# Kernel tuning notes

Hardware: AMD Instinct MI355X
Metric: run time of the kernel (lower is better)

## Reference

```python
import jax, jax.numpy as jnp
import numpy as np

H = 32  # hidden size

def _lstm_layer(x, Wih, Whh, bih, bhh):
    # x: [B, T, in]; Wih: [4H, in]; Whh: [4H, H]; biases: [4H]
    # Precompute input contribution for all timesteps (one big GEMM).
    xg = jnp.einsum('bti,gi->btg', x, Wih) + (bih + bhh)  # [B, T, 4H]
    B = x.shape[0]
    h0 = jnp.zeros((B, H), x.dtype)
    c0 = jnp.zeros((B, H), x.dtype)

    def step(carry, xt):
        h, c = carry
        g = xt + h @ Whh.T                      # [B, 4H]
        i, f, gg, o = jnp.split(g, 4, axis=-1)   # PyTorch gate order: i,f,g,o
        i = jax.nn.sigmoid(i)
        f = jax.nn.sigmoid(f)
        gg = jnp.tanh(gg)
        o = jax.nn.sigmoid(o)
        c = f * c + i * gg
        h = o * jnp.tanh(c)
        return (h, c), h

    (_, _), hs = jax.lax.scan(step, (h0, c0), jnp.swapaxes(xg, 0, 1))  # hs: [T, B, H]
    return jnp.swapaxes(hs, 0, 1)  # [B, T, H]


def setup_inputs() -> dict:
    key = jax.random.key(0)
    ks = jax.random.split(key, 11)
    B, T = 4096, 1024
    s = 1.0 / np.sqrt(H)  # PyTorch LSTM init scale
    f32 = jnp.float32
    return {
        'x':    jax.random.normal(ks[0], (B, T, 1), dtype=f32),
        'Wih0': jax.random.uniform(ks[1], (4 * H, 1), dtype=f32, minval=-s, maxval=s),
        'Whh0': jax.random.uniform(ks[2], (4 * H, H), dtype=f32, minval=-s, maxval=s),
        'bih0': jax.random.uniform(ks[3], (4 * H,), dtype=f32, minval=-s, maxval=s),
        'bhh0': jax.random.uniform(ks[4], (4 * H,), dtype=f32, minval=-s, maxval=s),
        'Wih1': jax.random.uniform(ks[5], (4 * H, H), dtype=f32, minval=-s, maxval=s),
        'Whh1': jax.random.uniform(ks[6], (4 * H, H), dtype=f32, minval=-s, maxval=s),
        'bih1': jax.random.uniform(ks[7], (4 * H,), dtype=f32, minval=-s, maxval=s),
        'bhh1': jax.random.uniform(ks[8], (4 * H,), dtype=f32, minval=-s, maxval=s),
        'Wfc':  jax.random.uniform(ks[9], (1, H), dtype=f32, minval=-s, maxval=s),
        'bfc':  jax.random.uniform(ks[10], (1,), dtype=f32, minval=-s, maxval=s),
    }


def reference(x, Wih0, Whh0, bih0, bhh0, Wih1, Whh1, bih1, bhh1, Wfc, bfc):
    h1 = _lstm_layer(x, Wih0, Whh0, bih0, bhh0)   # [B, T, H]
    h2 = _lstm_layer(h1, Wih1, Whh1, bih1, bhh1)  # [B, T, H]
    last = h2[:, -1, :]                            # [B, H]
    return last @ Wfc.T + bfc                      # [B, 1]
```

## Files before the change

kernel.cpp:

```cpp
#include <hip/hip_runtime.h>

#define HSZ  32
#define TLEN 1024
#define PS   40

typedef _Float16 half8 __attribute__((ext_vector_type(8)));
typedef float    f32x4 __attribute__((ext_vector_type(4)));

__device__ __forceinline__ float rcp_f(float x){ return __builtin_amdgcn_rcpf(x); }
__device__ __forceinline__ float exp2_f(float x){ return __builtin_amdgcn_exp2f(x); }
#define LOG2E 1.442695040888963f
__device__ __forceinline__ float sigmoid_f(float x){ return rcp_f(1.0f + exp2_f(-LOG2E*x)); }
__device__ __forceinline__ float tanh_fast(float x){ return 1.0f - 2.0f*rcp_f(1.0f + exp2_f(2.0f*LOG2E*x)); }
__device__ __forceinline__ f32x4 mfma16(half8 a, half8 b, f32x4 c){
  return __builtin_amdgcn_mfma_f32_16x16x32_f16(a, b, c, 0, 0, 0);
}

__device__ __forceinline__ void lds_barrier(){
  asm volatile("s_waitcnt lgkmcnt(0)\n\ts_barrier" ::: "memory");
}

__global__ __launch_bounds__(512, 2) void lstm2_mfma8(
    const float* __restrict__ x,
    const float* __restrict__ Wih0, const float* __restrict__ Whh0,
    const float* __restrict__ bih0, const float* __restrict__ bhh0,
    const float* __restrict__ Wih1, const float* __restrict__ Whh1,
    const float* __restrict__ bih1, const float* __restrict__ bhh1,
    const float* __restrict__ Wfc,  const float* __restrict__ bfc,
    float* __restrict__ out, int Tn)
{
  __shared__ __align__(16) _Float16 hpl[2][2][16*PS];

  const int tid = threadIdx.x;
  const int w   = tid >> 6;
  const int l   = tid & 63;
  const int col = l & 15;
  const int g   = l >> 4;
  const int s   = 4*w + g;
  const int b0  = blockIdx.x * 16;

  const int prow = 32*(col & 3) + 4*w + (col >> 2);
  half8 W0h, W0l, WIh, WIl, WHh, WHl;
  {
    const float* p0 = Whh0 + prow*HSZ + 8*g;
    const float* p1 = Wih1 + prow*HSZ + 8*g;
    const float* p2 = Whh1 + prow*HSZ + 8*g;
    #pragma unroll
    for (int j = 0; j < 8; ++j){
      float v0 = p0[j], v1 = p1[j], v2 = p2[j];
      _Float16 a = (_Float16)v0; W0h[j] = a; W0l[j] = (_Float16)(v0 - (float)a);
      _Float16 b = (_Float16)v1; WIh[j] = b; WIl[j] = (_Float16)(v1 - (float)b);
      _Float16 c = (_Float16)v2; WHh[j] = c; WHl[j] = (_Float16)(v2 - (float)c);
    }
  }
  float wx[4], bs0[4];
  f32x4 bias1;
  #pragma unroll
  for (int j = 0; j < 4; ++j){
    int r    = 32*j + s;
    wx[j]    = Wih0[r];
    bs0[j]   = bih0[r] + bhh0[r];
    bias1[j] = bih1[r] + bhh1[r];
  }
  const f32x4 zero4 = {0.f, 0.f, 0.f, 0.f};

  const int wrI = col*PS + s;
  const int rdI = col*PS + 8*g;

  for (int i = tid; i < 2*2*16*PS; i += 512) (&hpl[0][0][0])[i] = (_Float16)0.0f;

  const float* xp = x + (size_t)(b0 + col) * Tn;
  float c0, c1 = 0.f, h1v = 0.f;

  {
    float x0 = xp[0];
    float e0 = fmaf(x0, wx[0], bs0[0]);
    float e2 = fmaf(x0, wx[2], bs0[2]);
    float e3 = fmaf(x0, wx[3], bs0[3]);
    float i0 = sigmoid_f(e0);
    float g0 = tanh_fast(e2);
    float o0 = sigmoid_f(e3);
    c0 = i0 * g0;
    float h0 = o0 * tanh_fast(c0);
    __syncthreads();
    hpl[0][0][wrI] = (_Float16)h0;
  }
  __syncthreads();
  half8 Bh0 = *(const half8*)&hpl[0][0][rdI];
  half8 Bh1 = *(const half8*)&hpl[0][1][rdI];
  float xv = xp[1];

#define STEP(Q, TIDX)                                                      \
  {                                                                        \
    float xn = xp[(TIDX)];               \
    f32x4 e;                                                               \
    e[0] = fmaf(xv, wx[0], bs0[0]);                                        \
    e[1] = fmaf(xv, wx[1], bs0[1]);                                        \
    e[2] = fmaf(xv, wx[2], bs0[2]);                                        \
    e[3] = fmaf(xv, wx[3], bs0[3]);                                        \
    f32x4 u, vv;                                                           \
    __builtin_amdgcn_s_setprio(1);                                         \
    e  = mfma16(W0h, Bh0, e);                                              \
    u  = mfma16(WHh, Bh1, bias1);                                          \
    vv = mfma16(WIh, Bh0, zero4);                                          \
    e  = mfma16(W0l, Bh0, e);                                              \
    u  = mfma16(WHl, Bh1, u);                                              \
    vv = mfma16(WIl, Bh0, vv);                                             \
    __builtin_amdgcn_s_setprio(0);                                         \
                                                                \
    float i1 = sigmoid_f(u[0] + vv[0]), f1 = sigmoid_f(u[1] + vv[1]);      \
    float g1 = tanh_fast(u[2] + vv[2]), o1 = sigmoid_f(u[3] + vv[3]);      \
    c1 = fmaf(f1, c1, i1 * g1);                                            \
    h1v = o1 * tanh_fast(c1);                                              \
    hpl[(Q)][1][wrI] = (_Float16)h1v;                                      \
                                                              \
    float i0 = sigmoid_f(e[0]), f0 = sigmoid_f(e[1]);                      \
    float g0 = tanh_fast(e[2]), o0 = sigmoid_f(e[3]);                      \
    c0 = fmaf(f0, c0, i0 * g0);                                            \
    float h0 = o0 * tanh_fast(c0);                                         \
    hpl[(Q)][0][wrI] = (_Float16)h0;                                       \
    lds_barrier();                                                         \
    Bh0 = *(const half8*)&hpl[(Q)][0][rdI];                                \
    Bh1 = *(const half8*)&hpl[(Q)][1][rdI];                                \
    xv = xn;                                                               \
  }

  for (int T0 = 0; T0 < Tn; T0 += 4){
    STEP(1, T0 + 2);
    STEP(0, T0 + 3);
    STEP(1, (T0 + 4 < Tn) ? T0 + 4 : Tn - 1);
    STEP(0, (T0 + 5 < Tn) ? T0 + 5 : Tn - 1);
  }
#undef STEP

  __syncthreads();
  float* sc = (float*)&hpl[0][0][0];
  sc[s*17 + col] = h1v;
  __syncthreads();
  if (tid < 16){
    float acc = bfc[0];
    #pragma unroll 8
    for (int k = 0; k < HSZ; ++k) acc = fmaf(sc[k*17 + tid], Wfc[k], acc);
    out[b0 + tid] = acc;
  }
}

extern "C" void kernel_launch(void* const* d_in, const int* in_sizes, int n_in,
                              void* d_out, int out_size, void* d_ws, size_t ws_size,
                              hipStream_t stream) {
  const float* x    = (const float*)d_in[0];
  const float* Wih0 = (const float*)d_in[1];
  const float* Whh0 = (const float*)d_in[2];
  const float* bih0 = (const float*)d_in[3];
  const float* bhh0 = (const float*)d_in[4];
  const float* Wih1 = (const float*)d_in[5];
  const float* Whh1 = (const float*)d_in[6];
  const float* bih1 = (const float*)d_in[7];
  const float* bhh1 = (const float*)d_in[8];
  const float* Wfc  = (const float*)d_in[9];
  const float* bfc  = (const float*)d_in[10];
  float* out = (float*)d_out;

  const int Tn = TLEN;
  const int B  = in_sizes[0] / Tn;

  dim3 block(512);
  dim3 grid(B / 16);
  hipLaunchKernelGGL(lstm2_mfma8, grid, block, 0, stream,
                     x, Wih0, Whh0, bih0, bhh0, Wih1, Whh1, bih1, bhh1,
                     Wfc, bfc, out, Tn);
}
```

Measured before the change: 427.0 us.

## Fold activation scales into weights and share reciprocals across gate pairs

```diff
diff --git a/kernel.cpp b/kernel.cpp
--- a/kernel.cpp
+++ b/kernel.cpp
@@ -10,8 +10,8 @@
 __device__ __forceinline__ float rcp_f(float x){ return __builtin_amdgcn_rcpf(x); }
 __device__ __forceinline__ float exp2_f(float x){ return __builtin_amdgcn_exp2f(x); }
 #define LOG2E 1.442695040888963f
-__device__ __forceinline__ float sigmoid_f(float x){ return rcp_f(1.0f + exp2_f(-LOG2E*x)); }
-__device__ __forceinline__ float tanh_fast(float x){ return 1.0f - 2.0f*rcp_f(1.0f + exp2_f(2.0f*LOG2E*x)); }
+#define SCL_S (-1.442695040888963f)
+#define SCL_T ( 2.885390081777927f)
 __device__ __forceinline__ f32x4 mfma16(half8 a, half8 b, f32x4 c){
   return __builtin_amdgcn_mfma_f32_16x16x32_f16(a, b, c, 0, 0, 0);
 }
@@ -20,7 +20,7 @@
   asm volatile("s_waitcnt lgkmcnt(0)\n\ts_barrier" ::: "memory");
 }
 
-__global__ __launch_bounds__(512, 2) void lstm2_mfma8(
+__global__ __launch_bounds__(512, 2) void lstm2_mfma9(
     const float* __restrict__ x,
     const float* __restrict__ Wih0, const float* __restrict__ Whh0,
     const float* __restrict__ bih0, const float* __restrict__ bhh0,
@@ -40,6 +40,7 @@
   const int b0  = blockIdx.x * 16;
 
   const int prow = 32*(col & 3) + 4*w + (col >> 2);
+  const float sA = ((col & 3) == 2) ? SCL_T : SCL_S;
   half8 W0h, W0l, WIh, WIl, WHh, WHl;
   {
     const float* p0 = Whh0 + prow*HSZ + 8*g;
@@ -47,20 +48,21 @@
     const float* p2 = Whh1 + prow*HSZ + 8*g;
     #pragma unroll
     for (int j = 0; j < 8; ++j){
-      float v0 = p0[j], v1 = p1[j], v2 = p2[j];
+      float v0 = p0[j]*sA, v1 = p1[j]*sA, v2 = p2[j]*sA;
       _Float16 a = (_Float16)v0; W0h[j] = a; W0l[j] = (_Float16)(v0 - (float)a);
       _Float16 b = (_Float16)v1; WIh[j] = b; WIl[j] = (_Float16)(v1 - (float)b);
       _Float16 c = (_Float16)v2; WHh[j] = c; WHl[j] = (_Float16)(v2 - (float)c);
     }
   }
+  const float scj[4] = {SCL_S, SCL_S, SCL_T, SCL_S};
   float wx[4], bs0[4];
   f32x4 bias1;
   #pragma unroll
   for (int j = 0; j < 4; ++j){
     int r    = 32*j + s;
-    wx[j]    = Wih0[r];
-    bs0[j]   = bih0[r] + bhh0[r];
-    bias1[j] = bih1[r] + bhh1[r];
+    wx[j]    = Wih0[r] * scj[j];
+    bs0[j]   = (bih0[r] + bhh0[r]) * scj[j];
+    bias1[j] = (bih1[r] + bhh1[r]) * scj[j];
   }
   const f32x4 zero4 = {0.f, 0.f, 0.f, 0.f};
 
@@ -77,11 +79,12 @@
     float e0 = fmaf(x0, wx[0], bs0[0]);
     float e2 = fmaf(x0, wx[2], bs0[2]);
     float e3 = fmaf(x0, wx[3], bs0[3]);
-    float i0 = sigmoid_f(e0);
-    float g0 = tanh_fast(e2);
-    float o0 = sigmoid_f(e3);
+    float i0 = rcp_f(1.f + exp2_f(e0));
+    float g0 = fmaf(-2.f, rcp_f(1.f + exp2_f(e2)), 1.f);
+    float o0 = rcp_f(1.f + exp2_f(e3));
     c0 = i0 * g0;
-    float h0 = o0 * tanh_fast(c0);
+    float th = fmaf(-2.f, rcp_f(1.f + exp2_f(SCL_T * c0)), 1.f);
+    float h0 = o0 * th;
     __syncthreads();
     hpl[0][0][wrI] = (_Float16)h0;
   }
@@ -107,17 +110,36 @@
     u  = mfma16(WHl, Bh1, u);                                              \
     vv = mfma16(WIl, Bh0, vv);                                             \
     __builtin_amdgcn_s_setprio(0);                                         \
-                                                                \
-    float i1 = sigmoid_f(u[0] + vv[0]), f1 = sigmoid_f(u[1] + vv[1]);      \
-    float g1 = tanh_fast(u[2] + vv[2]), o1 = sigmoid_f(u[3] + vv[3]);      \
+                   \
+    float Zi = exp2_f(u[0] + vv[0]), Zf = exp2_f(u[1] + vv[1]);            \
+    float Zg = exp2_f(u[2] + vv[2]), Zo = exp2_f(u[3] + vv[3]);            \
+    float di = 1.f + Zi, df = 1.f + Zf, dg = 1.f + Zg, dq = 1.f + Zo;      \
+    float ra = rcp_f(di * df);                                             \
+    float i1 = ra * df, f1 = ra * di;                                      \
+    float rb = rcp_f(dg * dq);                                             \
+    float g1 = fmaf(-2.f, rb * dq, 1.f);                                   \
+    float o1 = rb * dg;                                                    \
     c1 = fmaf(f1, c1, i1 * g1);                                            \
-    h1v = o1 * tanh_fast(c1);                                              \
+    float Zc1 = exp2_f(SCL_T * c1);                                        \
+    float dc1 = 1.f + Zc1;                                                 \
+                                               \
+    float Xi = exp2_f(e[0]), Xf = exp2_f(e[1]);                            \
+    float Xg = exp2_f(e[2]), Xo = exp2_f(e[3]);                            \
+    float ei = 1.f + Xi, ef = 1.f + Xf, eg = 1.f + Xg, eq = 1.f + Xo;      \
+    float rc2 = rcp_f(ei * ef);                                            \
+    float i0 = rc2 * ef, f0 = rc2 * ei;                                    \
+    float rd2 = rcp_f(eg * eq);                                            \
+    float g0 = fmaf(-2.f, rd2 * eq, 1.f);                                  \
+    float o0 = rd2 * eg;                                                   \
+    c0 = fmaf(f0, c0, i0 * g0);                                            \
+    float Zc0 = exp2_f(SCL_T * c0);                                        \
+    float dc0 = 1.f + Zc0;                                                 \
+                                 \
+    float re = rcp_f(dc1 * dc0);                                           \
+    float t1 = re * dc0, t0 = re * dc1;                                    \
+    float q1 = t1 * o1; h1v = fmaf(-2.f, q1, o1);                          \
+    float q0 = t0 * o0; float h0 = fmaf(-2.f, q0, o0);                     \
     hpl[(Q)][1][wrI] = (_Float16)h1v;                                      \
-                                                              \
-    float i0 = sigmoid_f(e[0]), f0 = sigmoid_f(e[1]);                      \
-    float g0 = tanh_fast(e[2]), o0 = sigmoid_f(e[3]);                      \
-    c0 = fmaf(f0, c0, i0 * g0);                                            \
-    float h0 = o0 * tanh_fast(c0);                                         \
     hpl[(Q)][0][wrI] = (_Float16)h0;                                       \
     lds_barrier();                                                         \
     Bh0 = *(const half8*)&hpl[(Q)][0][rdI];                                \
@@ -166,7 +188,7 @@
 
   dim3 block(512);
   dim3 grid(B / 16);
-  hipLaunchKernelGGL(lstm2_mfma8, grid, block, 0, stream,
+  hipLaunchKernelGGL(lstm2_mfma9, grid, block, 0, stream,
                      x, Wih0, Whh0, bih0, bhh0, Wih1, Whh1, bih1, bhh1,
                      Wfc, bfc, out, Tn);
 }
```

New measurement: 420.0 us. No clear change (-1.6%).

## Split LSTM layers across warp groups as producer/consumer with paired activations

Applied to the files above, without the earlier changes.

```diff
diff --git a/kernel.cpp b/kernel.cpp
--- a/kernel.cpp
+++ b/kernel.cpp
@@ -9,18 +9,34 @@
 
 __device__ __forceinline__ float rcp_f(float x){ return __builtin_amdgcn_rcpf(x); }
 __device__ __forceinline__ float exp2_f(float x){ return __builtin_amdgcn_exp2f(x); }
-#define LOG2E 1.442695040888963f
-__device__ __forceinline__ float sigmoid_f(float x){ return rcp_f(1.0f + exp2_f(-LOG2E*x)); }
-__device__ __forceinline__ float tanh_fast(float x){ return 1.0f - 2.0f*rcp_f(1.0f + exp2_f(2.0f*LOG2E*x)); }
+#define SCL_S (-1.442695040888963f)
+#define SCL_T ( 2.885390081777927f)
+
 __device__ __forceinline__ f32x4 mfma16(half8 a, half8 b, f32x4 c){
   return __builtin_amdgcn_mfma_f32_16x16x32_f16(a, b, c, 0, 0, 0);
 }
-
 __device__ __forceinline__ void lds_barrier(){
   asm volatile("s_waitcnt lgkmcnt(0)\n\ts_barrier" ::: "memory");
 }
 
-__global__ __launch_bounds__(512, 2) void lstm2_mfma8(
+#define ACT4(A0,A1,A2,A3, CV, IV, FV, GV, OV)                  \
+  { float Zi_ = exp2_f(A0), Zf_ = exp2_f(A1);                  \
+    float Zg_ = exp2_f(A2), Zo_ = exp2_f(A3);                  \
+    float di_ = 1.f+Zi_, df_ = 1.f+Zf_;                        \
+    float dg_ = 1.f+Zg_, dq_ = 1.f+Zo_;                        \
+    float r1_ = rcp_f(di_*df_); IV = r1_*df_; FV = r1_*di_;    \
+    float r2_ = rcp_f(dg_*dq_);                                \
+    GV = fmaf(-2.f, r2_*dq_, 1.f); OV = r2_*dg_;               \
+    CV = fmaf(FV, CV, IV*GV); }
+
+#define TANHPAIR(CA, CB, OA, OB, HA, HB)                       \
+  { float ZA_ = exp2_f(SCL_T*(CA)), ZB_ = exp2_f(SCL_T*(CB));  \
+    float dA_ = 1.f+ZA_, dB_ = 1.f+ZB_;                        \
+    float re_ = rcp_f(dA_*dB_);                                \
+    float qA_ = re_*dB_*(OA), qB_ = re_*dA_*(OB);              \
+    HA = fmaf(-2.f, qA_, OA); HB = fmaf(-2.f, qB_, OB); }
+
+__global__ __launch_bounds__(512, 2) void lstm2_pc(
     const float* __restrict__ x,
     const float* __restrict__ Wih0, const float* __restrict__ Whh0,
     const float* __restrict__ bih0, const float* __restrict__ bhh0,
@@ -36,106 +52,164 @@
   const int l   = tid & 63;
   const int col = l & 15;
   const int g   = l >> 4;
-  const int s   = 4*w + g;
+  const int wl  = w & 3;
   const int b0  = blockIdx.x * 16;
-
-  const int prow = 32*(col & 3) + 4*w + (col >> 2);
-  half8 W0h, W0l, WIh, WIl, WHh, WHl;
-  {
-    const float* p0 = Whh0 + prow*HSZ + 8*g;
-    const float* p1 = Wih1 + prow*HSZ + 8*g;
-    const float* p2 = Whh1 + prow*HSZ + 8*g;
-    #pragma unroll
-    for (int j = 0; j < 8; ++j){
-      float v0 = p0[j], v1 = p1[j], v2 = p2[j];
-      _Float16 a = (_Float16)v0; W0h[j] = a; W0l[j] = (_Float16)(v0 - (float)a);
-      _Float16 b = (_Float16)v1; WIh[j] = b; WIl[j] = (_Float16)(v1 - (float)b);
-      _Float16 c = (_Float16)v2; WHh[j] = c; WHl[j] = (_Float16)(v2 - (float)c);
-    }
-  }
-  float wx[4], bs0[4];
-  f32x4 bias1;
+  const bool isL0 = (w < 4);
+
+  const int rdI = col*PS + 8*g;
+  const int wrA = col*PS + 8*wl + g;
+  const int wrB = wrA + 4;
+  const float sA = ((col & 3) == 2) ? SCL_T : SCL_S;
+  const float scj[4] = {SCL_S, SCL_S, SCL_T, SCL_S};
+  const f32x4 zero4 = {0.f, 0.f, 0.f, 0.f};
+
+  for (int i = tid; i < 2*2*16*PS; i += 512) (&hpl[0][0][0])[i] = (_Float16)0.0f;
+
+  float wxA[4], wxB[4], bsA[4], bsB[4];
   #pragma unroll
   for (int j = 0; j < 4; ++j){
-    int r    = 32*j + s;
-    wx[j]    = Wih0[r];
-    bs0[j]   = bih0[r] + bhh0[r];
-    bias1[j] = bih1[r] + bhh1[r];
-  }
-  const f32x4 zero4 = {0.f, 0.f, 0.f, 0.f};
-
-  const int wrI = col*PS + s;
-  const int rdI = col*PS + 8*g;
-
-  for (int i = tid; i < 2*2*16*PS; i += 512) (&hpl[0][0][0])[i] = (_Float16)0.0f;
-
+    int rA = 32*j + 8*wl + g, rB = rA + 4;
+    wxA[j] = Wih0[rA] * scj[j];
+    wxB[j] = Wih0[rB] * scj[j];
+    bsA[j] = (bih0[rA] + bhh0[rA]) * scj[j];
+    bsB[j] = (bih1 == bih1 ? (bih0[rB] + bhh0[rB]) : 0.f) * scj[j];
+  }
   const float* xp = x + (size_t)(b0 + col) * Tn;
-  float c0, c1 = 0.f, h1v = 0.f;
-
-  {
+
+  __syncthreads();
+
+  if (isL0){
     float x0 = xp[0];
-    float e0 = fmaf(x0, wx[0], bs0[0]);
-    float e2 = fmaf(x0, wx[2], bs0[2]);
-    float e3 = fmaf(x0, wx[3], bs0[3]);
-    float i0 = sigmoid_f(e0);
-    float g0 = tanh_fast(e2);
-    float o0 = sigmoid_f(e3);
-    c0 = i0 * g0;
-    float h0 = o0 * tanh_fast(c0);
-    __syncthreads();
-    hpl[0][0][wrI] = (_Float16)h0;
-  }
-  __syncthreads();
-  half8 Bh0 = *(const half8*)&hpl[0][0][rdI];
-  half8 Bh1 = *(const half8*)&hpl[0][1][rdI];
-  float xv = xp[1];
-
-#define STEP(Q, TIDX)                                                      \
-  {                                                                        \
-    float xn = xp[(TIDX)];               \
-    f32x4 e;                                                               \
-    e[0] = fmaf(xv, wx[0], bs0[0]);                                        \
-    e[1] = fmaf(xv, wx[1], bs0[1]);                                        \
-    e[2] = fmaf(xv, wx[2], bs0[2]);                                        \
-    e[3] = fmaf(xv, wx[3], bs0[3]);                                        \
-    f32x4 u, vv;                                                           \
-    __builtin_amdgcn_s_setprio(1);                                         \
-    e  = mfma16(W0h, Bh0, e);                                              \
-    u  = mfma16(WHh, Bh1, bias1);                                          \
-    vv = mfma16(WIh, Bh0, zero4);                                          \
-    e  = mfma16(W0l, Bh0, e);                                              \
-    u  = mfma16(WHl, Bh1, u);                                              \
-    vv = mfma16(WIl, Bh0, vv);                                             \
-    __builtin_amdgcn_s_setprio(0);                                         \
-                                                                \
-    float i1 = sigmoid_f(u[0] + vv[0]), f1 = sigmoid_f(u[1] + vv[1]);      \
-    float g1 = tanh_fast(u[2] + vv[2]), o1 = sigmoid_f(u[3] + vv[3]);      \
-    c1 = fmaf(f1, c1, i1 * g1);                                            \
-    h1v = o1 * tanh_fast(c1);                                              \
-    hpl[(Q)][1][wrI] = (_Float16)h1v;                                      \
-                                                              \
-    float i0 = sigmoid_f(e[0]), f0 = sigmoid_f(e[1]);                      \
-    float g0 = tanh_fast(e[2]), o0 = sigmoid_f(e[3]);                      \
-    c0 = fmaf(f0, c0, i0 * g0);                                            \
-    float h0 = o0 * tanh_fast(c0);                                         \
-    hpl[(Q)][0][wrI] = (_Float16)h0;                                       \
-    lds_barrier();                                                         \
-    Bh0 = *(const half8*)&hpl[(Q)][0][rdI];                                \
-    Bh1 = *(const half8*)&hpl[(Q)][1][rdI];                                \
-    xv = xn;                                                               \
-  }
-
-  for (int T0 = 0; T0 < Tn; T0 += 4){
-    STEP(1, T0 + 2);
-    STEP(0, T0 + 3);
-    STEP(1, (T0 + 4 < Tn) ? T0 + 4 : Tn - 1);
-    STEP(0, (T0 + 5 < Tn) ? T0 + 5 : Tn - 1);
-  }
-#undef STEP
+    float c0A = 0.f, c0B = 0.f, iA,fA,gA,oA, iB,fB,gB,oB, h0A, h0B;
+    ACT4(fmaf(x0,wxA[0],bsA[0]), fmaf(x0,wxA[1],bsA[1]),
+         fmaf(x0,wxA[2],bsA[2]), fmaf(x0,wxA[3],bsA[3]), c0A, iA,fA,gA,oA);
+    ACT4(fmaf(x0,wxB[0],bsB[0]), fmaf(x0,wxB[1],bsB[1]),
+         fmaf(x0,wxB[2],bsB[2]), fmaf(x0,wxB[3],bsB[3]), c0B, iB,fB,gB,oB);
+    TANHPAIR(c0A, c0B, oA, oB, h0A, h0B);
+    hpl[0][0][wrA] = (_Float16)h0A;
+    hpl[0][0][wrB] = (_Float16)h0B;
+    wxA[0] = wxA[0];
+    ;
+  }
+  __syncthreads();
+
+  float h1Av = 0.f, h1Bv = 0.f;
+
+  if (isL0){
+    const int prowA = 32*(col & 3) + 8*wl + (col >> 2);
+    half8 WhA, WlA, WhB, WlB;
+    {
+      const float* pA = Whh0 + prowA*HSZ + 8*g;
+      const float* pB = pA + 4*HSZ;
+      #pragma unroll
+      for (int j = 0; j < 8; ++j){
+        float vA = pA[j]*sA, vB = pB[j]*sA;
+        _Float16 a = (_Float16)vA; WhA[j] = a; WlA[j] = (_Float16)(vA - (float)a);
+        _Float16 b = (_Float16)vB; WhB[j] = b; WlB[j] = (_Float16)(vB - (float)b);
+      }
+    }
+    float c0A = 0.f, c0B = 0.f;
+    {
+      float x0 = xp[0];
+      float iA,fA,gA,oA, iB,fB,gB,oB;
+      ACT4(fmaf(x0,wxA[0],bsA[0]), fmaf(x0,wxA[1],bsA[1]),
+           fmaf(x0,wxA[2],bsA[2]), fmaf(x0,wxA[3],bsA[3]), c0A, iA,fA,gA,oA);
+      ACT4(fmaf(x0,wxB[0],bsB[0]), fmaf(x0,wxB[1],bsB[1]),
+           fmaf(x0,wxB[2],bsB[2]), fmaf(x0,wxB[3],bsB[3]), c0B, iB,fB,gB,oB);
+    }
+    half8 Bh0 = *(const half8*)&hpl[0][0][rdI];
+    float xv = xp[1];
+
+#define L0STEP(Q, XNI)                                                     \
+    {                                                                      \
+      float xn = xp[(XNI)];                                                \
+      f32x4 eA, eB;                                                        \
+      eA[0]=fmaf(xv,wxA[0],bsA[0]); eA[1]=fmaf(xv,wxA[1],bsA[1]);          \
+      eA[2]=fmaf(xv,wxA[2],bsA[2]); eA[3]=fmaf(xv,wxA[3],bsA[3]);          \
+      eB[0]=fmaf(xv,wxB[0],bsB[0]); eB[1]=fmaf(xv,wxB[1],bsB[1]);          \
+      eB[2]=fmaf(xv,wxB[2],bsB[2]); eB[3]=fmaf(xv,wxB[3],bsB[3]);          \
+      __builtin_amdgcn_s_setprio(1);                                       \
+      eA = mfma16(WhA, Bh0, eA);  eB = mfma16(WhB, Bh0, eB);               \
+      eA = mfma16(WlA, Bh0, eA);  eB = mfma16(WlB, Bh0, eB);               \
+      __builtin_amdgcn_s_setprio(0);                                       \
+      float iA,fA,gA,oA, iB,fB,gB,oB, h0A, h0B;                            \
+      ACT4(eA[0],eA[1],eA[2],eA[3], c0A, iA,fA,gA,oA);                     \
+      ACT4(eB[0],eB[1],eB[2],eB[3], c0B, iB,fB,gB,oB);                     \
+      TANHPAIR(c0A, c0B, oA, oB, h0A, h0B);                                \
+      hpl[(Q)][0][wrA] = (_Float16)h0A;                                    \
+      hpl[(Q)][0][wrB] = (_Float16)h0B;                                    \
+      lds_barrier();                                                       \
+      Bh0 = *(const half8*)&hpl[(Q)][0][rdI];                              \
+      xv = xn;                                                             \
+    }
+
+    for (int T0 = 0; T0 < Tn; T0 += 2){
+      L0STEP(1, (T0+2 < Tn) ? T0+2 : Tn-1);
+      L0STEP(0, (T0+3 < Tn) ? T0+3 : Tn-1);
+    }
+#undef L0STEP
+  } else {
+    const int prowA = 32*(col & 3) + 8*wl + (col >> 2);
+    half8 WIhA, WIlA, WIhB, WIlB, WHhA, WHlA, WHhB, WHlB;
+    {
+      const float* iA_ = Wih1 + prowA*HSZ + 8*g;
+      const float* iB_ = iA_ + 4*HSZ;
+      const float* hA_ = Whh1 + prowA*HSZ + 8*g;
+      const float* hB_ = hA_ + 4*HSZ;
+      #pragma unroll
+      for (int j = 0; j < 8; ++j){
+        float v0 = iA_[j]*sA, v1 = iB_[j]*sA, v2 = hA_[j]*sA, v3 = hB_[j]*sA;
+        _Float16 a = (_Float16)v0; WIhA[j] = a; WIlA[j] = (_Float16)(v0 - (float)a);
+        _Float16 b = (_Float16)v1; WIhB[j] = b; WIlB[j] = (_Float16)(v1 - (float)b);
+        _Float16 c = (_Float16)v2; WHhA[j] = c; WHlA[j] = (_Float16)(v2 - (float)c);
+        _Float16 d = (_Float16)v3; WHhB[j] = d; WHlB[j] = (_Float16)(v3 - (float)d);
+      }
+    }
+    f32x4 bias1A, bias1B;
+    #pragma unroll
+    for (int j = 0; j < 4; ++j){
+      int rA = 32*j + 8*wl + g, rB = rA + 4;
+      bias1A[j] = (bih1[rA] + bhh1[rA]) * scj[j];
+      bias1B[j] = (bih1[rB] + bhh1[rB]) * scj[j];
+    }
+    float c1A = 0.f, c1B = 0.f;
+    half8 Bh0 = *(const half8*)&hpl[0][0][rdI];
+    half8 Bh1 = *(const half8*)&hpl[0][1][rdI];
+
+#define L1STEP(Q)                                                          \
+    {                                                                      \
+      f32x4 uA, uB, vvA, vvB;                                              \
+      __builtin_amdgcn_s_setprio(1);                                       \
+      uA  = mfma16(WHhA, Bh1, bias1A);  uB  = mfma16(WHhB, Bh1, bias1B);   \
+      vvA = mfma16(WIhA, Bh0, zero4);   vvB = mfma16(WIhB, Bh0, zero4);    \
+      uA  = mfma16(WHlA, Bh1, uA);      uB  = mfma16(WHlB, Bh1, uB);       \
+      vvA = mfma16(WIlA, Bh0, vvA);     vvB = mfma16(WIlB, Bh0, vvB);      \
+      __builtin_amdgcn_s_setprio(0);                                       \
+      f32x4 aA = uA + vvA, aB = uB + vvB;                                  \
+      float iA,fA,gA,oA, iB,fB,gB,oB;                                      \
+      ACT4(aA[0],aA[1],aA[2],aA[3], c1A, iA,fA,gA,oA);                     \
+      ACT4(aB[0],aB[1],aB[2],aB[3], c1B, iB,fB,gB,oB);                     \
+      TANHPAIR(c1A, c1B, oA, oB, h1Av, h1Bv);                              \
+      hpl[(Q)][1][wrA] = (_Float16)h1Av;                                   \
+      hpl[(Q)][1][wrB] = (_Float16)h1Bv;                                   \
+      lds_barrier();                                                       \
+      Bh0 = *(const half8*)&hpl[(Q)][0][rdI];                              \
+      Bh1 = *(const half8*)&hpl[(Q)][1][rdI];                              \
+    }
+
+    for (int T0 = 0; T0 < Tn; T0 += 2){
+      L1STEP(1);
+      L1STEP(0);
+    }
+#undef L1STEP
+  }
 
   __syncthreads();
   float* sc = (float*)&hpl[0][0][0];
-  sc[s*17 + col] = h1v;
+  if (w >= 4){
+    sc[(8*wl + g)*17 + col]     = h1Av;
+    sc[(8*wl + 4 + g)*17 + col] = h1Bv;
+  }
   __syncthreads();
   if (tid < 16){
     float acc = bfc[0];
@@ -166,7 +240,7 @@
 
   dim3 block(512);
   dim3 grid(B / 16);
-  hipLaunchKernelGGL(lstm2_mfma8, grid, block, 0, stream,
+  hipLaunchKernelGGL(lstm2_pc, grid, block, 0, stream,
                      x, Wih0, Whh0, bih0, bhh0, Wih1, Whh1, bih1, bhh1,
                      Wfc, bfc, out, Tn);
 }
```

Result: faster. 411.8 us (-3.6%).

## Halve block to 4 waves with two hidden units per lane and fused activations

Applied to the files above, without the earlier changes.

```diff
diff --git a/kernel.cpp b/kernel.cpp
--- a/kernel.cpp
+++ b/kernel.cpp
@@ -2,25 +2,45 @@
 
 #define HSZ  32
 #define TLEN 1024
-#define PS   40
 
 typedef _Float16 half8 __attribute__((ext_vector_type(8)));
 typedef float    f32x4 __attribute__((ext_vector_type(4)));
 
 __device__ __forceinline__ float rcp_f(float x){ return __builtin_amdgcn_rcpf(x); }
 __device__ __forceinline__ float exp2_f(float x){ return __builtin_amdgcn_exp2f(x); }
-#define LOG2E 1.442695040888963f
-__device__ __forceinline__ float sigmoid_f(float x){ return rcp_f(1.0f + exp2_f(-LOG2E*x)); }
-__device__ __forceinline__ float tanh_fast(float x){ return 1.0f - 2.0f*rcp_f(1.0f + exp2_f(2.0f*LOG2E*x)); }
+#define SCL_S (-1.442695040888963f)
+#define SCL_T ( 2.885390081777927f)
+
 __device__ __forceinline__ f32x4 mfma16(half8 a, half8 b, f32x4 c){
   return __builtin_amdgcn_mfma_f32_16x16x32_f16(a, b, c, 0, 0, 0);
 }
-
 __device__ __forceinline__ void lds_barrier(){
   asm volatile("s_waitcnt lgkmcnt(0)\n\ts_barrier" ::: "memory");
 }
+__device__ __forceinline__ unsigned int packh2(float a, float b){
+  _Float16 ha = (_Float16)a, hb = (_Float16)b;
+  return (unsigned int)__builtin_bit_cast(unsigned short, ha)
+       | ((unsigned int)__builtin_bit_cast(unsigned short, hb) << 16);
+}
 
-__global__ __launch_bounds__(512, 2) void lstm2_mfma8(
+#define ACT4(A0,A1,A2,A3, CV, IV, FV, GV, OV)                  \
+  { float Zi_ = exp2_f(A0), Zf_ = exp2_f(A1);                  \
+    float Zg_ = exp2_f(A2), Zo_ = exp2_f(A3);                  \
+    float di_ = 1.f+Zi_, df_ = 1.f+Zf_;                        \
+    float dg_ = 1.f+Zg_, dq_ = 1.f+Zo_;                        \
+    float r1_ = rcp_f(di_*df_); IV = r1_*df_; FV = r1_*di_;    \
+    float r2_ = rcp_f(dg_*dq_);                                \
+    GV = fmaf(-2.f, r2_*dq_, 1.f); OV = r2_*dg_;               \
+    CV = fmaf(FV, CV, IV*GV); }
+
+#define TANHPAIR(CA, CB, OA, OB, HA, HB)                       \
+  { float ZA_ = exp2_f(SCL_T*(CA)), ZB_ = exp2_f(SCL_T*(CB));  \
+    float dA_ = 1.f+ZA_, dB_ = 1.f+ZB_;                        \
+    float re_ = rcp_f(dA_*dB_);                                \
+    float qA_ = re_*dB_*(OA), qB_ = re_*dA_*(OB);              \
+    HA = fmaf(-2.f, qA_, OA); HB = fmaf(-2.f, qB_, OB); }
+
+__global__ __launch_bounds__(256, 1) void lstm2_slot(
     const float* __restrict__ x,
     const float* __restrict__ Wih0, const float* __restrict__ Whh0,
     const float* __restrict__ bih0, const float* __restrict__ bhh0,
@@ -29,113 +49,120 @@
     const float* __restrict__ Wfc,  const float* __restrict__ bfc,
     float* __restrict__ out, int Tn)
 {
-  __shared__ __align__(16) _Float16 hpl[2][2][16*PS];
+  __shared__ __align__(16) _Float16 hx[2][2][1024];
 
   const int tid = threadIdx.x;
   const int w   = tid >> 6;
   const int l   = tid & 63;
-  const int col = l & 15;
+  const int c   = l & 15;
   const int g   = l >> 4;
-  const int s   = 4*w + g;
+  const int ta  = 2*w, tb = 2*w + 1;
   const int b0  = blockIdx.x * 16;
+  const int Pc  = 32*(c & 3) + 8*(c >> 2);
+  const float sA = ((c & 3) == 2) ? SCL_T : SCL_S;
+  const float scj[4] = {SCL_S, SCL_S, SCL_T, SCL_S};
+  const f32x4 zero4 = {0.f, 0.f, 0.f, 0.f};
+  const int rdI = (g*16 + c)*8;
+  const int wrI = rdI + ta;
 
-  const int prow = 32*(col & 3) + 4*w + (col >> 2);
-  half8 W0h, W0l, WIh, WIl, WHh, WHl;
-  {
-    const float* p0 = Whh0 + prow*HSZ + 8*g;
-    const float* p1 = Wih1 + prow*HSZ + 8*g;
-    const float* p2 = Whh1 + prow*HSZ + 8*g;
+  for (int i = tid; i < 2*2*1024; i += 256) (&hx[0][0][0])[i] = (_Float16)0.0f;
+
+  half8 W0h[2], W0l[2], WHh[2], WHl[2], WIh[2], WIl[2];
+  #pragma unroll
+  for (int tt = 0; tt < 2; ++tt){
+    const int pr = Pc + ta + tt;
+    const float* p0 = Whh0 + pr*HSZ + 8*g;
+    const float* p1 = Whh1 + pr*HSZ + 8*g;
+    const float* p2 = Wih1 + pr*HSZ + 8*g;
     #pragma unroll
     for (int j = 0; j < 8; ++j){
-      float v0 = p0[j], v1 = p1[j], v2 = p2[j];
-      _Float16 a = (_Float16)v0; W0h[j] = a; W0l[j] = (_Float16)(v0 - (float)a);
-      _Float16 b = (_Float16)v1; WIh[j] = b; WIl[j] = (_Float16)(v1 - (float)b);
-      _Float16 c = (_Float16)v2; WHh[j] = c; WHl[j] = (_Float16)(v2 - (float)c);
+      float v0 = p0[j]*sA, v1 = p1[j]*sA, v2 = p2[j]*sA;
+      _Float16 a = (_Float16)v0; W0h[tt][j] = a; W0l[tt][j] = (_Float16)(v0 - (float)a);
+      _Float16 b = (_Float16)v1; WHh[tt][j] = b; WHl[tt][j] = (_Float16)(v1 - (float)b);
+      _Float16 d = (_Float16)v2; WIh[tt][j] = d; WIl[tt][j] = (_Float16)(v2 - (float)d);
     }
   }
-  float wx[4], bs0[4];
-  f32x4 bias1;
+  float wx[2][4], bs0[2][4];
+  f32x4 bias1[2];
   #pragma unroll
-  for (int j = 0; j < 4; ++j){
-    int r    = 32*j + s;
-    wx[j]    = Wih0[r];
-    bs0[j]   = bih0[r] + bhh0[r];
-    bias1[j] = bih1[r] + bhh1[r];
+  for (int tt = 0; tt < 2; ++tt){
+    #pragma unroll
+    for (int j = 0; j < 4; ++j){
+      int r = 32*j + 8*g + ta + tt;
+      wx[tt][j]   = Wih0[r] * scj[j];
+      bs0[tt][j]  = (bih0[r] + bhh0[r]) * scj[j];
+      bias1[tt][j] = (bih1[r] + bhh1[r]) * scj[j];
+    }
   }
-  const f32x4 zero4 = {0.f, 0.f, 0.f, 0.f};
 
-  const int wrI = col*PS + s;
-  const int rdI = col*PS + 8*g;
+  const float* xp = x + (size_t)(b0 + c) * Tn;
+  float c0a = 0.f, c0b = 0.f, c1a = 0.f, c1b = 0.f;
+  float h1a = 0.f, h1b = 0.f;
 
-  for (int i = tid; i < 2*2*16*PS; i += 512) (&hpl[0][0][0])[i] = (_Float16)0.0f;
-
-  const float* xp = x + (size_t)(b0 + col) * Tn;
-  float c0, c1 = 0.f, h1v = 0.f;
+  __syncthreads();
 
   {
     float x0 = xp[0];
-    float e0 = fmaf(x0, wx[0], bs0[0]);
-    float e2 = fmaf(x0, wx[2], bs0[2]);
-    float e3 = fmaf(x0, wx[3], bs0[3]);
-    float i0 = sigmoid_f(e0);
-    float g0 = tanh_fast(e2);
-    float o0 = sigmoid_f(e3);
-    c0 = i0 * g0;
-    float h0 = o0 * tanh_fast(c0);
-    __syncthreads();
-    hpl[0][0][wrI] = (_Float16)h0;
+    float iva,fva,gva,ova, ivb,fvb,gvb,ovb, h0a, h0b;
+    ACT4(fmaf(x0,wx[0][0],bs0[0][0]), fmaf(x0,wx[0][1],bs0[0][1]),
+         fmaf(x0,wx[0][2],bs0[0][2]), fmaf(x0,wx[0][3],bs0[0][3]),
+         c0a, iva,fva,gva,ova);
+    ACT4(fmaf(x0,wx[1][0],bs0[1][0]), fmaf(x0,wx[1][1],bs0[1][1]),
+         fmaf(x0,wx[1][2],bs0[1][2]), fmaf(x0,wx[1][3],bs0[1][3]),
+         c0b, ivb,fvb,gvb,ovb);
+    TANHPAIR(c0a, c0b, ova, ovb, h0a, h0b);
+    *(unsigned int*)&hx[0][0][wrI] = packh2(h0a, h0b);
   }
   __syncthreads();
-  half8 Bh0 = *(const half8*)&hpl[0][0][rdI];
-  half8 Bh1 = *(const half8*)&hpl[0][1][rdI];
+  half8 Bh0 = *(const half8*)&hx[0][0][rdI];
+  half8 Bh1 = *(const half8*)&hx[0][1][rdI];
   float xv = xp[1];
 
-#define STEP(Q, TIDX)                                                      \
+#define STEP(Q, XNI)                                                       \
   {                                                                        \
-    float xn = xp[(TIDX)];               \
-    f32x4 e;                                                               \
-    e[0] = fmaf(xv, wx[0], bs0[0]);                                        \
-    e[1] = fmaf(xv, wx[1], bs0[1]);                                        \
-    e[2] = fmaf(xv, wx[2], bs0[2]);                                        \
-    e[3] = fmaf(xv, wx[3], bs0[3]);                                        \
-    f32x4 u, vv;                                                           \
-    __builtin_amdgcn_s_setprio(1);                                         \
-    e  = mfma16(W0h, Bh0, e);                                              \
-    u  = mfma16(WHh, Bh1, bias1);                                          \
-    vv = mfma16(WIh, Bh0, zero4);                                          \
-    e  = mfma16(W0l, Bh0, e);                                              \
-    u  = mfma16(WHl, Bh1, u);                                              \
-    vv = mfma16(WIl, Bh0, vv);                                             \
-    __builtin_amdgcn_s_setprio(0);                                         \
+    float xn = xp[(XNI)];                                                  \
+    f32x4 e0, e1;                                                          \
+    e0[0]=fmaf(xv,wx[0][0],bs0[0][0]); e0[1]=fmaf(xv,wx[0][1],bs0[0][1]);  \
+    e0[2]=fmaf(xv,wx[0][2],bs0[0][2]); e0[3]=fmaf(xv,wx[0][3],bs0[0][3]);  \
+    e1[0]=fmaf(xv,wx[1][0],bs0[1][0]); e1[1]=fmaf(xv,wx[1][1],bs0[1][1]);  \
+    e1[2]=fmaf(xv,wx[1][2],bs0[1][2]); e1[3]=fmaf(xv,wx[1][3],bs0[1][3]);  \
+    f32x4 u0 = mfma16(WHh[0], Bh1, bias1[0]);                              \
+    f32x4 u1 = mfma16(WHh[1], Bh1, bias1[1]);                              \
+    f32x4 v0 = mfma16(WIh[0], Bh0, zero4);                                 \
+    f32x4 v1 = mfma16(WIh[1], Bh0, zero4);                                 \
+    e0 = mfma16(W0h[0], Bh0, e0);  e1 = mfma16(W0h[1], Bh0, e1);           \
+    u0 = mfma16(WHl[0], Bh1, u0);  u1 = mfma16(WHl[1], Bh1, u1);           \
+    v0 = mfma16(WIl[0], Bh0, v0);  v1 = mfma16(WIl[1], Bh0, v1);           \
+    e0 = mfma16(W0l[0], Bh0, e0);  e1 = mfma16(W0l[1], Bh0, e1);           \
+    f32x4 a0 = u0 + v0, a1 = u1 + v1;                                      \
                                                                 \
-    float i1 = sigmoid_f(u[0] + vv[0]), f1 = sigmoid_f(u[1] + vv[1]);      \
-    float g1 = tanh_fast(u[2] + vv[2]), o1 = sigmoid_f(u[3] + vv[3]);      \
-    c1 = fmaf(f1, c1, i1 * g1);                                            \
-    h1v = o1 * tanh_fast(c1);                                              \
-    hpl[(Q)][1][wrI] = (_Float16)h1v;                                      \
+    float i1a,f1a,g1a,o1a, i1b,f1b,g1b,o1b;                                \
+    ACT4(a0[0],a0[1],a0[2],a0[3], c1a, i1a,f1a,g1a,o1a);                   \
+    ACT4(a1[0],a1[1],a1[2],a1[3], c1b, i1b,f1b,g1b,o1b);                   \
+    TANHPAIR(c1a, c1b, o1a, o1b, h1a, h1b);                                \
+    *(unsigned int*)&hx[(Q)][1][wrI] = packh2(h1a, h1b);                   \
                                                               \
-    float i0 = sigmoid_f(e[0]), f0 = sigmoid_f(e[1]);                      \
-    float g0 = tanh_fast(e[2]), o0 = sigmoid_f(e[3]);                      \
-    c0 = fmaf(f0, c0, i0 * g0);                                            \
-    float h0 = o0 * tanh_fast(c0);                                         \
-    hpl[(Q)][0][wrI] = (_Float16)h0;                                       \
+    float i0a,f0a,g0a,o0a, i0b,f0b,g0b,o0b, h0a, h0b;                      \
+    ACT4(e0[0],e0[1],e0[2],e0[3], c0a, i0a,f0a,g0a,o0a);                   \
+    ACT4(e1[0],e1[1],e1[2],e1[3], c0b, i0b,f0b,g0b,o0b);                   \
+    TANHPAIR(c0a, c0b, o0a, o0b, h0a, h0b);                                \
+    *(unsigned int*)&hx[(Q)][0][wrI] = packh2(h0a, h0b);                   \
     lds_barrier();                                                         \
-    Bh0 = *(const half8*)&hpl[(Q)][0][rdI];                                \
-    Bh1 = *(const half8*)&hpl[(Q)][1][rdI];                                \
+    Bh0 = *(const half8*)&hx[(Q)][0][rdI];                                 \
+    Bh1 = *(const half8*)&hx[(Q)][1][rdI];                                 \
     xv = xn;                                                               \
   }
 
-  for (int T0 = 0; T0 < Tn; T0 += 4){
-    STEP(1, T0 + 2);
-    STEP(0, T0 + 3);
-    STEP(1, (T0 + 4 < Tn) ? T0 + 4 : Tn - 1);
-    STEP(0, (T0 + 5 < Tn) ? T0 + 5 : Tn - 1);
+  for (int T0 = 0; T0 < Tn; T0 += 2){
+    STEP(1, (T0+2 < Tn) ? T0+2 : Tn-1);
+    STEP(0, (T0+3 < Tn) ? T0+3 : Tn-1);
   }
 #undef STEP
 
   __syncthreads();
-  float* sc = (float*)&hpl[0][0][0];
-  sc[s*17 + col] = h1v;
+  float* sc = (float*)&hx[0][0][0];
+  sc[(8*g + ta)*17 + c] = h1a;
+  sc[(8*g + tb)*17 + c] = h1b;
   __syncthreads();
   if (tid < 16){
     float acc = bfc[0];
@@ -164,9 +191,9 @@
   const int Tn = TLEN;
   const int B  = in_sizes[0] / Tn;
 
-  dim3 block(512);
+  dim3 block(256);
   dim3 grid(B / 16);
-  hipLaunchKernelGGL(lstm2_mfma8, grid, block, 0, stream,
+  hipLaunchKernelGGL(lstm2_slot, grid, block, 0, stream,
                      x, Wih0, Whh0, bih0, bhh0, Wih1, Whh1, bih1, bhh1,
                      Wfc, bfc, out, Tn);
 }
```

Measured after the change: 479.8 us. 1.12x slower.
